# Optimization experiments

Hardware: AMD Instinct MI355X
Metric: run time of the kernel (lower is better)

## Reference

```python
import jax, jax.numpy as jnp
import numpy as np

N = 100000
E = 1600000
C = 128
NEG_SLOPE = 0.2
BN_EPS = 1e-5


def setup_inputs() -> dict:
    key = jax.random.key(0)
    ks = jax.random.split(key, 6)
    x = jax.random.normal(ks[0], (N, C), dtype=jnp.float32)
    edge_index = jax.random.randint(ks[1], (2, E), 0, N, dtype=jnp.int64)
    # Glorot-ish scaled params, stacked over the 3 layers (all 128->128)
    Ws = jax.random.normal(ks[2], (3, C, C), dtype=jnp.float32) * (1.0 / np.sqrt(C))
    att_srcs = jax.random.normal(ks[3], (3, C), dtype=jnp.float32) * (1.0 / np.sqrt(C))
    att_dsts = jax.random.normal(ks[4], (3, C), dtype=jnp.float32) * (1.0 / np.sqrt(C))
    biases = jnp.zeros((3, C), dtype=jnp.float32)
    gammas = jnp.ones((3, C), dtype=jnp.float32)
    betas = jnp.zeros((3, C), dtype=jnp.float32)
    return {"x": x, "edge_index": edge_index, "Ws": Ws, "att_srcs": att_srcs,
            "att_dsts": att_dsts, "biases": biases, "gammas": gammas, "betas": betas}


def _gat_layer(x, W, a_src, a_dst, bias, src, dst):
    # linear transform: [N, C]
    h = x @ W
    # per-node attention logits
    s_src = h @ a_src  # [N]
    s_dst = h @ a_dst  # [N]
    # edge-wise gather + leaky relu scoring
    e = jax.nn.leaky_relu(s_src[src] + s_dst[dst], NEG_SLOPE)  # [E+N]
    # scatter-softmax over incoming edges of each target node
    m = jax.ops.segment_max(e, dst, num_segments=N)  # every node has a self-loop
    ex = jnp.exp(e - m[dst])
    denom = jax.ops.segment_sum(ex, dst, num_segments=N)
    alpha = ex / denom[dst]  # [E+N]
    # scatter-add aggregation of alpha-weighted source features
    out = jax.ops.segment_sum(alpha[:, None] * h[src], dst, num_segments=N)
    return out + bias


def _batch_norm(x, gamma, beta):
    mu = jnp.mean(x, axis=0)
    var = jnp.mean(jnp.square(x - mu), axis=0)
    return gamma * (x - mu) * jax.lax.rsqrt(var + BN_EPS) + beta


def reference(x, edge_index, Ws, att_srcs, att_dsts, biases, gammas, betas):
    # PyG GATConv adds self-loops by default
    loops = jnp.arange(N, dtype=edge_index.dtype)
    src = jnp.concatenate([edge_index[0], loops])
    dst = jnp.concatenate([edge_index[1], loops])
    outs = []
    for l in range(3):
        x = _gat_layer(x, Ws[l], att_srcs[l], att_dsts[l], biases[l], src, dst)
        x = jax.nn.relu(x)
        x = _batch_norm(x, gammas[l], betas[l])
        outs.append(x)
    # jump=True: concat all layer outputs -> [N, 3*C]
    return jnp.concatenate(outs, axis=-1)
```

## Files before the change

### kernel.cpp

```cpp
#include <hip/hip_runtime.h>
#include <math.h>

#define N_NODES 100000
#define N_EDGES 1600000
#define M_TOT   (N_EDGES + N_NODES)
#define C_DIM   128
#define NEG_SLOPE 0.2f
#define BN_EPS 1e-5f

#define NBUCK 8
#define BUCK_NODES 12500
#define BUCK_CAP 240000

#define KS2 72
#define BN_NB 256
#define SCAN_NB 98

typedef _Float16 f16x8 __attribute__((ext_vector_type(8)));
typedef float f32x4 __attribute__((ext_vector_type(4)));

static __device__ __forceinline__ unsigned short f2h(float f) {
    _Float16 h = (_Float16)f;
    unsigned short u;
    __builtin_memcpy(&u, &h, 2);
    return u;
}
static __device__ __forceinline__ float h2f(unsigned short u) {
    _Float16 h;
    __builtin_memcpy(&h, &u, 2);
    return (float)h;
}

__global__ void zero_i32(int* __restrict__ p, int n) {
    int i = blockIdx.x * blockDim.x + threadIdx.x;
    if (i < n) p[i] = 0;
}

__global__ __launch_bounds__(256) void bucket_edges(const int* __restrict__ ei,
                                                    int* __restrict__ bucket_next,
                                                    int2* __restrict__ buckets) {
    __shared__ int cnt[NBUCK];
    __shared__ int base[NBUCK];
    int tid = threadIdx.x;
    if (tid < NBUCK) cnt[tid] = 0;
    __syncthreads();
    int m = blockIdx.x * 256 + tid;
    int src = 0, dst = 0, p = 0, myoff = 0;
    bool valid = (m < M_TOT);
    if (valid) {
        if (m < N_EDGES) { src = ei[m]; dst = ei[N_EDGES + m]; }
        else             { src = m - N_EDGES; dst = src; }
        p = dst / BUCK_NODES;
        myoff = atomicAdd(&cnt[p], 1);
    }
    __syncthreads();
    if (tid < NBUCK) base[tid] = (cnt[tid] > 0) ? atomicAdd(&bucket_next[tid], cnt[tid]) : 0;
    __syncthreads();
    if (valid) {
        buckets[(size_t)p * BUCK_CAP + base[p] + myoff] = make_int2(src, dst);
    }
}

__global__ __launch_bounds__(256) void count_deg_b(const int2* __restrict__ buckets,
                                                   const int* __restrict__ bucket_next,
                                                   int* __restrict__ deg) {
    int p = blockIdx.x & 7;
    int chunk = blockIdx.x >> 3;
    int len = bucket_next[p];
    const int2* b = buckets + (size_t)p * BUCK_CAP;
    int stride = (gridDim.x >> 3) * 256;
    for (int i = chunk * 256 + threadIdx.x; i < len; i += stride) {
        atomicAdd(&deg[b[i].y], 1);
    }
}

__global__ __launch_bounds__(256) void scatter_b(const int2* __restrict__ buckets,
                                                 const int* __restrict__ bucket_next,
                                                 int* __restrict__ nextp,
                                                 int* __restrict__ csr_src) {
    int p = blockIdx.x & 7;
    int chunk = blockIdx.x >> 3;
    int len = bucket_next[p];
    const int2* b = buckets + (size_t)p * BUCK_CAP;
    int stride = (gridDim.x >> 3) * 256;
    for (int i = chunk * 256 + threadIdx.x; i < len; i += stride) {
        int2 e = b[i];
        int pos = atomicAdd(&nextp[e.y], 1);
        csr_src[pos] = e.x;
    }
}

__global__ __launch_bounds__(256) void block_sums(const int* __restrict__ deg,
                                                  int* __restrict__ partials) {
    __shared__ int lds[256];
    int base = blockIdx.x * 1024;
    int s = 0;
    for (int i = threadIdx.x; i < 1024; i += 256) {
        int idx = base + i;
        if (idx < N_NODES) s += deg[idx];
    }
    lds[threadIdx.x] = s;
    __syncthreads();
    for (int off = 128; off > 0; off >>= 1) {
        if (threadIdx.x < off) lds[threadIdx.x] += lds[threadIdx.x + off];
        __syncthreads();
    }
    if (threadIdx.x == 0) partials[blockIdx.x] = lds[0];
}

__global__ __launch_bounds__(128) void scan_partials(int* __restrict__ partials, int nb,
                                                     int* __restrict__ row_ptr) {
    __shared__ int lds[128];
    int tid = threadIdx.x;
    int v = (tid < nb) ? partials[tid] : 0;
    lds[tid] = v;
    __syncthreads();
    for (int off = 1; off < 128; off <<= 1) {
        int t = (tid >= off) ? lds[tid - off] : 0;
        __syncthreads();
        lds[tid] += t;
        __syncthreads();
    }
    if (tid < nb) partials[tid] = lds[tid] - v;
    if (tid == 0) row_ptr[N_NODES] = M_TOT;
}

__global__ __launch_bounds__(256) void scan_write(const int* __restrict__ deg,
                                                  const int* __restrict__ partials,
                                                  int* __restrict__ row_ptr,
                                                  int* __restrict__ nextp) {
    __shared__ int lds[256];
    int tid = threadIdx.x;
    int base = blockIdx.x * 1024;
    int i0 = base + tid * 4;
    int d[4];
#pragma unroll
    for (int t = 0; t < 4; ++t)
        d[t] = (i0 + t < N_NODES) ? deg[i0 + t] : 0;
    int tsum = d[0] + d[1] + d[2] + d[3];
    lds[tid] = tsum;
    __syncthreads();
    for (int off = 1; off < 256; off <<= 1) {
        int v = (tid >= off) ? lds[tid - off] : 0;
        __syncthreads();
        lds[tid] += v;
        __syncthreads();
    }
    int excl = lds[tid] - tsum;
    int run = partials[blockIdx.x] + excl;
#pragma unroll
    for (int t = 0; t < 4; ++t) {
        if (i0 + t < N_NODES) {
            row_ptr[i0 + t] = run;
            nextp[i0 + t]   = run;
            run += d[t];
        }
    }
}

__global__ __launch_bounds__(256, 3) void gemm_attn(
    const float* __restrict__ X, int ldx,
    const float* __restrict__ W,
    const float* __restrict__ a_src, const float* __restrict__ a_dst,
    const float* __restrict__ gbv,
    float* __restrict__ outw,
    unsigned short* __restrict__ Hh, float* __restrict__ Ssrc,
    float* __restrict__ Sdst) {
    __shared__ unsigned short Xs[128 * KS2];
    __shared__ unsigned short Wt[128 * KS2];
    int tid = threadIdx.x;
    int rbase = blockIdx.x * 128;

    int wave = tid >> 6;
    int lane = tid & 63;
    int q = lane >> 4;
    int l15 = lane & 15;
    int wrow = wave * 32;

    f32x4 acc[2][8] = {};

    for (int kb = 0; kb < 128; kb += 64) {
        __syncthreads();
        {
            int rl = tid >> 4;
            int cg = (tid & 15) * 4;
            float4 gg = make_float4(1.f, 1.f, 1.f, 1.f);
            float4 bb = make_float4(0.f, 0.f, 0.f, 0.f);
            if (gbv) {
                gg = *(const float4*)&gbv[kb + cg];
                bb = *(const float4*)&gbv[128 + kb + cg];
            }
#pragma unroll
            for (int i = 0; i < 8; ++i) {
                int r = rl + i * 16;
                int row0 = rbase + r;
                bool ok = (row0 < N_NODES);
                int row = ok ? row0 : (N_NODES - 1);
                float4 v = *(const float4*)&X[(size_t)row * ldx + kb + cg];
                if (gbv) {
                    v.x = fmaf(v.x, gg.x, bb.x);
                    v.y = fmaf(v.y, gg.y, bb.y);
                    v.z = fmaf(v.z, gg.z, bb.z);
                    v.w = fmaf(v.w, gg.w, bb.w);
                    if (ok) *(float4*)&outw[(size_t)row * 384 + kb + cg] = v;
                }
                ushort4 o;
                o.x = f2h(v.x); o.y = f2h(v.y); o.z = f2h(v.z); o.w = f2h(v.w);
                *(ushort4*)&Xs[r * KS2 + cg] = o;
            }
        }
        {
            int kl = tid >> 5;
            int n4 = (tid & 31) * 4;
#pragma unroll
            for (int i = 0; i < 8; ++i) {
                int kk = kl + i * 8;
                float4 v = *(const float4*)&W[(kb + kk) * 128 + n4];
                Wt[(n4 + 0) * KS2 + kk] = f2h(v.x);
                Wt[(n4 + 1) * KS2 + kk] = f2h(v.y);
                Wt[(n4 + 2) * KS2 + kk] = f2h(v.z);
                Wt[(n4 + 3) * KS2 + kk] = f2h(v.w);
            }
        }
        __syncthreads();
#pragma unroll
        for (int ks = 0; ks < 64; ks += 32) {
            int k0 = ks + q * 8;
            f16x8 a0 = *(f16x8*)&Xs[(wrow + l15) * KS2 + k0];
            f16x8 a1 = *(f16x8*)&Xs[(wrow + 16 + l15) * KS2 + k0];
#pragma unroll
            for (int c = 0; c < 8; ++c) {
                f16x8 b = *(f16x8*)&Wt[(c * 16 + l15) * KS2 + k0];
                acc[0][c] = __builtin_amdgcn_mfma_f32_16x16x32_f16(a0, b, acc[0][c], 0, 0, 0);
                acc[1][c] = __builtin_amdgcn_mfma_f32_16x16x32_f16(a1, b, acc[1][c], 0, 0, 0);
            }
        }
    }

    float avs[8], avd[8];
#pragma unroll
    for (int c = 0; c < 8; ++c) {
        avs[c] = a_src[c * 16 + l15];
        avd[c] = a_dst[c * 16 + l15];
    }
#pragma unroll
    for (int r = 0; r < 2; ++r) {
        float ps[4] = {0, 0, 0, 0}, pd[4] = {0, 0, 0, 0};
#pragma unroll
        for (int g = 0; g < 4; ++g) {
            int row = rbase + wrow + r * 16 + q * 4 + g;
            bool ok = (row < N_NODES);
#pragma unroll
            for (int c = 0; c < 8; ++c) {
                float h = acc[r][c][g];
                if (ok) Hh[(size_t)row * 128 + c * 16 + l15] = f2h(h);
                ps[g] = fmaf(h, avs[c], ps[g]);
                pd[g] = fmaf(h, avd[c], pd[g]);
            }
        }
#pragma unroll
        for (int g = 0; g < 4; ++g) {
#pragma unroll
            for (int off = 1; off < 16; off <<= 1) {
                ps[g] += __shfl_xor(ps[g], off, 64);
                pd[g] += __shfl_xor(pd[g], off, 64);
            }
        }
        if (l15 == 0) {
#pragma unroll
            for (int g = 0; g < 4; ++g) {
                int row = rbase + wrow + r * 16 + q * 4 + g;
                if (row < N_NODES) {
                    Ssrc[row] = ps[g];
                    Sdst[row] = pd[g];
                }
            }
        }
    }
}

__global__ __launch_bounds__(256) void aggregate(
    const unsigned short* __restrict__ Hh, const int* __restrict__ row_ptr,
    const int* __restrict__ csr_src,
    const float* __restrict__ Ssrc, const float* __restrict__ Sdst,
    const float* __restrict__ bias, float* __restrict__ Y) {
    int wave = threadIdx.x >> 6;
    int lane = threadIdx.x & 63;
    int g = lane >> 4;
    int l15 = lane & 15;
    int v = blockIdx.x * 4 + wave;
    int start = row_ptr[v];
    int end = row_ptr[v + 1];
    float sdv = Sdst[v];

    float sself = Ssrc[v] + sdv;
    float m = (sself > 0.0f) ? sself : NEG_SLOPE * sself;

    float acc[8] = {0, 0, 0, 0, 0, 0, 0, 0};
    float denom = 0.0f;

    int j = start;
    for (; j + 16 <= end; j += 16) {
        int u0 = csr_src[j + g];
        int u1 = csr_src[j + 4 + g];
        int u2 = csr_src[j + 8 + g];
        int u3 = csr_src[j + 12 + g];
        float ss0 = Ssrc[u0];
        float ss1 = Ssrc[u1];
        float ss2 = Ssrc[u2];
        float ss3 = Ssrc[u3];
        f16x8 h0 = *(const f16x8*)&Hh[(size_t)u0 * 128 + l15 * 8];
        f16x8 h1 = *(const f16x8*)&Hh[(size_t)u1 * 128 + l15 * 8];
        f16x8 h2 = *(const f16x8*)&Hh[(size_t)u2 * 128 + l15 * 8];
        f16x8 h3 = *(const f16x8*)&Hh[(size_t)u3 * 128 + l15 * 8];
        float s0 = ss0 + sdv; s0 = (s0 > 0.0f) ? s0 : NEG_SLOPE * s0;
        float s1 = ss1 + sdv; s1 = (s1 > 0.0f) ? s1 : NEG_SLOPE * s1;
        float s2 = ss2 + sdv; s2 = (s2 > 0.0f) ? s2 : NEG_SLOPE * s2;
        float s3 = ss3 + sdv; s3 = (s3 > 0.0f) ? s3 : NEG_SLOPE * s3;
        float w0 = __expf(s0 - m);
        float w1 = __expf(s1 - m);
        float w2 = __expf(s2 - m);
        float w3 = __expf(s3 - m);
        denom += (w0 + w1) + (w2 + w3);
#pragma unroll
        for (int i = 0; i < 8; ++i) acc[i] = fmaf(w0, (float)h0[i], acc[i]);
#pragma unroll
        for (int i = 0; i < 8; ++i) acc[i] = fmaf(w1, (float)h1[i], acc[i]);
#pragma unroll
        for (int i = 0; i < 8; ++i) acc[i] = fmaf(w2, (float)h2[i], acc[i]);
#pragma unroll
        for (int i = 0; i < 8; ++i) acc[i] = fmaf(w3, (float)h3[i], acc[i]);
    }
    for (; j + 8 <= end; j += 8) {
        int u0 = csr_src[j + g];
        int u1 = csr_src[j + 4 + g];
        float ss0 = Ssrc[u0];
        float ss1 = Ssrc[u1];
        f16x8 h0 = *(const f16x8*)&Hh[(size_t)u0 * 128 + l15 * 8];
        f16x8 h1 = *(const f16x8*)&Hh[(size_t)u1 * 128 + l15 * 8];
        float s0 = ss0 + sdv; s0 = (s0 > 0.0f) ? s0 : NEG_SLOPE * s0;
        float s1 = ss1 + sdv; s1 = (s1 > 0.0f) ? s1 : NEG_SLOPE * s1;
        float w0 = __expf(s0 - m);
        float w1 = __expf(s1 - m);
        denom += w0 + w1;
#pragma unroll
        for (int i = 0; i < 8; ++i) acc[i] = fmaf(w0, (float)h0[i], acc[i]);
#pragma unroll
        for (int i = 0; i < 8; ++i) acc[i] = fmaf(w1, (float)h1[i], acc[i]);
    }
    for (; j < end; j += 4) {
        int je = j + g;
        bool ok = (je < end);
        int u = ok ? csr_src[je] : v;
        float s = Ssrc[u] + sdv; s = (s > 0.0f) ? s : NEG_SLOPE * s;
        float w = ok ? __expf(s - m) : 0.0f;
        f16x8 h = *(const f16x8*)&Hh[(size_t)u * 128 + l15 * 8];
        denom += w;
#pragma unroll
        for (int i = 0; i < 8; ++i) acc[i] = fmaf(w, (float)h[i], acc[i]);
    }

#pragma unroll
    for (int i = 0; i < 8; ++i) {
        acc[i] += __shfl_xor(acc[i], 16, 64);
        acc[i] += __shfl_xor(acc[i], 32, 64);
    }
    denom += __shfl_xor(denom, 16, 64);
    denom += __shfl_xor(denom, 32, 64);

    if (g == 0) {
        float inv = 1.0f / denom;
        float4 b0 = *(const float4*)&bias[l15 * 8];
        float4 b1 = *(const float4*)&bias[l15 * 8 + 4];
        float4 o0, o1;
        o0.x = fmaxf(fmaf(acc[0], inv, b0.x), 0.0f);
        o0.y = fmaxf(fmaf(acc[1], inv, b0.y), 0.0f);
        o0.z = fmaxf(fmaf(acc[2], inv, b0.z), 0.0f);
        o0.w = fmaxf(fmaf(acc[3], inv, b0.w), 0.0f);
        o1.x = fmaxf(fmaf(acc[4], inv, b1.x), 0.0f);
        o1.y = fmaxf(fmaf(acc[5], inv, b1.y), 0.0f);
        o1.z = fmaxf(fmaf(acc[6], inv, b1.z), 0.0f);
        o1.w = fmaxf(fmaf(acc[7], inv, b1.w), 0.0f);
        *(float4*)&Y[(size_t)v * 128 + l15 * 8] = o0;
        *(float4*)&Y[(size_t)v * 128 + l15 * 8 + 4] = o1;
    }
}

__global__ __launch_bounds__(256) void bn_stats(const float* __restrict__ Y,
                                                float* __restrict__ partial) {
    __shared__ float red[256 * 8];
    int tid = threadIdx.x;
    int rowlane = tid >> 5;
    int cg = tid & 31;
    float4 s = make_float4(0, 0, 0, 0);
    float4 qq = make_float4(0, 0, 0, 0);
    for (int i = blockIdx.x * 8 + rowlane; i < N_NODES; i += BN_NB * 8) {
        float4 v = *(const float4*)&Y[(size_t)i * 128 + cg * 4];
        s.x += v.x; s.y += v.y; s.z += v.z; s.w += v.w;
        qq.x = fmaf(v.x, v.x, qq.x);
        qq.y = fmaf(v.y, v.y, qq.y);
        qq.z = fmaf(v.z, v.z, qq.z);
        qq.w = fmaf(v.w, v.w, qq.w);
    }
    float* r = &red[tid * 8];
    r[0] = s.x; r[1] = s.y; r[2] = s.z; r[3] = s.w;
    r[4] = qq.x; r[5] = qq.y; r[6] = qq.z; r[7] = qq.w;
    __syncthreads();
    for (int off = 4; off > 0; off >>= 1) {
        if (rowlane < off) {
            float* o = &red[(tid + off * 32) * 8];
#pragma unroll
            for (int t = 0; t < 8; ++t) r[t] += o[t];
        }
        __syncthreads();
    }
    if (rowlane == 0) {
        *(float4*)&partial[(size_t)blockIdx.x * 256 + cg * 4] =
            make_float4(r[0], r[1], r[2], r[3]);
        *(float4*)&partial[(size_t)blockIdx.x * 256 + 128 + cg * 4] =
            make_float4(r[4], r[5], r[6], r[7]);
    }
}

__global__ __launch_bounds__(256) void bn_finalize(const float* __restrict__ partial,
                                                   const float* __restrict__ gamma,
                                                   const float* __restrict__ beta,
                                                   float* __restrict__ gb) {
    __shared__ float tot[256];
    int tid = threadIdx.x;
    float acc = 0.0f;
    for (int b = 0; b < BN_NB; ++b) acc += partial[(size_t)b * 256 + tid];
    tot[tid] = acc;
    __syncthreads();
    if (tid < 128) {
        const float invN = 1.0f / (float)N_NODES;
        float mu = tot[tid] * invN;
        float var = tot[128 + tid] * invN - mu * mu;
        float g = gamma[tid] * rsqrtf(var + BN_EPS);
        gb[tid] = g;
        gb[128 + tid] = beta[tid] - mu * g;
    }
}

__global__ __launch_bounds__(256) void bn_apply(const float* __restrict__ Y,
                                                const float* __restrict__ gb,
                                                float* __restrict__ out) {
    int idx = blockIdx.x * blockDim.x + threadIdx.x;
    if (idx >= N_NODES * 32) return;
    int row = idx >> 5;
    int c4 = (idx & 31) * 4;
    float4 v = *(const float4*)&Y[(size_t)row * 128 + c4];
    float4 g = *(const float4*)&gb[c4];
    float4 b = *(const float4*)&gb[128 + c4];
    v.x = fmaf(v.x, g.x, b.x);
    v.y = fmaf(v.y, g.y, b.y);
    v.z = fmaf(v.z, g.z, b.z);
    v.w = fmaf(v.w, g.w, b.w);
    *(float4*)&out[(size_t)row * 384 + c4] = v;
}

extern "C" void kernel_launch(void* const* d_in, const int* in_sizes, int n_in,
                              void* d_out, int out_size, void* d_ws, size_t ws_size,
                              hipStream_t stream) {
    const float* x      = (const float*)d_in[0];
    const int*   ei     = (const int*)d_in[1];
    const float* Wall   = (const float*)d_in[2];
    const float* asrcs  = (const float*)d_in[3];
    const float* adsts  = (const float*)d_in[4];
    const float* biases = (const float*)d_in[5];
    const float* gammas = (const float*)d_in[6];
    const float* betas  = (const float*)d_in[7];
    float* out = (float*)d_out;

    unsigned short* Hh = (unsigned short*)d_ws;
    float* Y       = (float*)(Hh + (size_t)N_NODES * 128);
    float* Ssrc    = Y + (size_t)N_NODES * 128;
    float* Sdst    = Ssrc + N_NODES;
    float* bnpart  = Sdst + N_NODES;
    float* gb      = bnpart + BN_NB * 256;
    int* deg       = (int*)(gb + 256);
    int* bucket_next = deg + N_NODES;
    int* row_ptr   = bucket_next + NBUCK;
    int* nextp     = row_ptr + (N_NODES + 1);
    int* partials  = nextp + N_NODES;
    int* csr_src   = partials + 128;
    int2* buckets  = (int2*)(csr_src + M_TOT + 2);

    const int ZERO_CNT = N_NODES + NBUCK;
    const int NB_EDGE = (M_TOT + 255) / 256;
    const int NB_PART = 2048;

    zero_i32<<<(ZERO_CNT + 255) / 256, 256, 0, stream>>>(deg, ZERO_CNT);
    bucket_edges<<<NB_EDGE, 256, 0, stream>>>(ei, bucket_next, buckets);
    count_deg_b<<<NB_PART, 256, 0, stream>>>(buckets, bucket_next, deg);
    block_sums<<<SCAN_NB, 256, 0, stream>>>(deg, partials);
    scan_partials<<<1, 128, 0, stream>>>(partials, SCAN_NB, row_ptr);
    scan_write<<<SCAN_NB, 256, 0, stream>>>(deg, partials, row_ptr, nextp);
    scatter_b<<<NB_PART, 256, 0, stream>>>(buckets, bucket_next, nextp, csr_src);

    for (int l = 0; l < 3; ++l) {
        const float* xin;
        int ldx;
        const float* gbl;
        float* outw;
        if (l == 0) { xin = x; ldx = 128; gbl = nullptr; outw = nullptr; }
        else        { xin = Y; ldx = 128; gbl = gb; outw = out + (size_t)(l - 1) * 128; }
        gemm_attn<<<(N_NODES + 127) / 128, 256, 0, stream>>>(
            xin, ldx, Wall + (size_t)l * 128 * 128,
            asrcs + l * 128, adsts + l * 128, gbl, outw, Hh, Ssrc, Sdst);
        aggregate<<<N_NODES / 4, 256, 0, stream>>>(
            Hh, row_ptr, csr_src, Ssrc, Sdst, biases + l * 128, Y);
        bn_stats<<<BN_NB, 256, 0, stream>>>(Y, bnpart);
        bn_finalize<<<1, 256, 0, stream>>>(bnpart, gammas + l * 128,
                                           betas + l * 128, gb);
    }
    bn_apply<<<(N_NODES * 32 + 255) / 256, 256, 0, stream>>>(
        Y, gb, out + (size_t)2 * 128);
}
```

Before: 803.8 us.

## Pre-convert weights to fp16 and feed MFMA operands directly from global memory

Adds a one-time kernel that converts all three weight matrices to transposed fp16. The GEMM then drops its LDS staging and barriers: each lane loads its X rows straight from global memory into MFMA A-fragments, applying the batch-norm affine inline, and reads B-fragments from the prepacked fp16 weights. This removes shared-memory traffic, the per-block W conversion and transposition, and the synchronisation. In exchange, W reads hit L2/L1 for every wave rather than being reused from LDS, the X loads are less coalesced, and the occupancy hint drops from 3 to 2.

```diff
diff --git a/kernel.cpp b/kernel.cpp
--- a/kernel.cpp
+++ b/kernel.cpp
@@ -12,7 +12,6 @@
 #define BUCK_NODES 12500
 #define BUCK_CAP 240000
 
-#define KS2 72
 #define BN_NB 256
 #define SCAN_NB 98
 
@@ -30,10 +29,22 @@
     __builtin_memcpy(&h, &u, 2);
     return (float)h;
 }
+static __device__ __forceinline__ _Float16 f2h16(float f) { return (_Float16)f; }
 
 __global__ void zero_i32(int* __restrict__ p, int n) {
     int i = blockIdx.x * blockDim.x + threadIdx.x;
     if (i < n) p[i] = 0;
+}
+
+__global__ __launch_bounds__(256) void conv_w(const float* __restrict__ Wall,
+                                              unsigned short* __restrict__ Wh) {
+    int i = blockIdx.x * 256 + threadIdx.x;
+    if (i >= 3 * 128 * 128) return;
+    int l = i >> 14;
+    int r = i & 16383;
+    int k = r >> 7;
+    int n = r & 127;
+    Wh[(size_t)l * 16384 + n * 128 + k] = f2h(Wall[i]);
 }
 
 __global__ __launch_bounds__(256) void bucket_edges(const int* __restrict__ ei,
@@ -158,82 +169,69 @@
     }
 }
 
-__global__ __launch_bounds__(256, 3) void gemm_attn(
+__global__ __launch_bounds__(256, 2) void gemm_attn(
     const float* __restrict__ X, int ldx,
-    const float* __restrict__ W,
+    const unsigned short* __restrict__ Wh,
     const float* __restrict__ a_src, const float* __restrict__ a_dst,
     const float* __restrict__ gbv,
     float* __restrict__ outw,
     unsigned short* __restrict__ Hh, float* __restrict__ Ssrc,
     float* __restrict__ Sdst) {
-    __shared__ unsigned short Xs[128 * KS2];
-    __shared__ unsigned short Wt[128 * KS2];
     int tid = threadIdx.x;
-    int rbase = blockIdx.x * 128;
-
     int wave = tid >> 6;
     int lane = tid & 63;
     int q = lane >> 4;
     int l15 = lane & 15;
     int wrow = wave * 32;
+    int rbase = blockIdx.x * 128;
+
+    int row0 = rbase + wrow + l15;
+    int row1 = row0 + 16;
+    bool ok0 = row0 < N_NODES, ok1 = row1 < N_NODES;
+    int r0c = ok0 ? row0 : (N_NODES - 1);
+    int r1c = ok1 ? row1 : (N_NODES - 1);
 
     f32x4 acc[2][8] = {};
 
-    for (int kb = 0; kb < 128; kb += 64) {
-        __syncthreads();
-        {
-            int rl = tid >> 4;
-            int cg = (tid & 15) * 4;
-            float4 gg = make_float4(1.f, 1.f, 1.f, 1.f);
-            float4 bb = make_float4(0.f, 0.f, 0.f, 0.f);
-            if (gbv) {
-                gg = *(const float4*)&gbv[kb + cg];
-                bb = *(const float4*)&gbv[128 + kb + cg];
+#pragma unroll
+    for (int ks = 0; ks < 128; ks += 32) {
+        int k0 = ks + q * 8;
+        float4 v0 = *(const float4*)&X[(size_t)r0c * ldx + k0];
+        float4 v1 = *(const float4*)&X[(size_t)r0c * ldx + k0 + 4];
+        float4 u0 = *(const float4*)&X[(size_t)r1c * ldx + k0];
+        float4 u1 = *(const float4*)&X[(size_t)r1c * ldx + k0 + 4];
+        if (gbv) {
+            float4 g0 = *(const float4*)&gbv[k0];
+            float4 g1 = *(const float4*)&gbv[k0 + 4];
+            float4 b0 = *(const float4*)&gbv[128 + k0];
+            float4 b1 = *(const float4*)&gbv[128 + k0 + 4];
+            v0.x = fmaf(v0.x, g0.x, b0.x); v0.y = fmaf(v0.y, g0.y, b0.y);
+            v0.z = fmaf(v0.z, g0.z, b0.z); v0.w = fmaf(v0.w, g0.w, b0.w);
+            v1.x = fmaf(v1.x, g1.x, b1.x); v1.y = fmaf(v1.y, g1.y, b1.y);
+            v1.z = fmaf(v1.z, g1.z, b1.z); v1.w = fmaf(v1.w, g1.w, b1.w);
+            u0.x = fmaf(u0.x, g0.x, b0.x); u0.y = fmaf(u0.y, g0.y, b0.y);
+            u0.z = fmaf(u0.z, g0.z, b0.z); u0.w = fmaf(u0.w, g0.w, b0.w);
+            u1.x = fmaf(u1.x, g1.x, b1.x); u1.y = fmaf(u1.y, g1.y, b1.y);
+            u1.z = fmaf(u1.z, g1.z, b1.z); u1.w = fmaf(u1.w, g1.w, b1.w);
+            if (ok0) {
+                *(float4*)&outw[(size_t)row0 * 384 + k0] = v0;
+                *(float4*)&outw[(size_t)row0 * 384 + k0 + 4] = v1;
             }
-#pragma unroll
-            for (int i = 0; i < 8; ++i) {
-                int r = rl + i * 16;
-                int row0 = rbase + r;
-                bool ok = (row0 < N_NODES);
-                int row = ok ? row0 : (N_NODES - 1);
-                float4 v = *(const float4*)&X[(size_t)row * ldx + kb + cg];
-                if (gbv) {
-                    v.x = fmaf(v.x, gg.x, bb.x);
-                    v.y = fmaf(v.y, gg.y, bb.y);
-                    v.z = fmaf(v.z, gg.z, bb.z);
-                    v.w = fmaf(v.w, gg.w, bb.w);
-                    if (ok) *(float4*)&outw[(size_t)row * 384 + kb + cg] = v;
-                }
-                ushort4 o;
-                o.x = f2h(v.x); o.y = f2h(v.y); o.z = f2h(v.z); o.w = f2h(v.w);
-                *(ushort4*)&Xs[r * KS2 + cg] = o;
+            if (ok1) {
+                *(float4*)&outw[(size_t)row1 * 384 + k0] = u0;
+                *(float4*)&outw[(size_t)row1 * 384 + k0 + 4] = u1;
             }
         }
-        {
-            int kl = tid >> 5;
-            int n4 = (tid & 31) * 4;
-#pragma unroll
-            for (int i = 0; i < 8; ++i) {
-                int kk = kl + i * 8;
-                float4 v = *(const float4*)&W[(kb + kk) * 128 + n4];
-                Wt[(n4 + 0) * KS2 + kk] = f2h(v.x);
-                Wt[(n4 + 1) * KS2 + kk] = f2h(v.y);
-                Wt[(n4 + 2) * KS2 + kk] = f2h(v.z);
-                Wt[(n4 + 3) * KS2 + kk] = f2h(v.w);
-            }
-        }
-        __syncthreads();
-#pragma unroll
-        for (int ks = 0; ks < 64; ks += 32) {
-            int k0 = ks + q * 8;
-            f16x8 a0 = *(f16x8*)&Xs[(wrow + l15) * KS2 + k0];
-            f16x8 a1 = *(f16x8*)&Xs[(wrow + 16 + l15) * KS2 + k0];
-#pragma unroll
-            for (int c = 0; c < 8; ++c) {
-                f16x8 b = *(f16x8*)&Wt[(c * 16 + l15) * KS2 + k0];
-                acc[0][c] = __builtin_amdgcn_mfma_f32_16x16x32_f16(a0, b, acc[0][c], 0, 0, 0);
-                acc[1][c] = __builtin_amdgcn_mfma_f32_16x16x32_f16(a1, b, acc[1][c], 0, 0, 0);
-            }
+        f16x8 a0, a1;
+        a0[0] = f2h16(v0.x); a0[1] = f2h16(v0.y); a0[2] = f2h16(v0.z); a0[3] = f2h16(v0.w);
+        a0[4] = f2h16(v1.x); a0[5] = f2h16(v1.y); a0[6] = f2h16(v1.z); a0[7] = f2h16(v1.w);
+        a1[0] = f2h16(u0.x); a1[1] = f2h16(u0.y); a1[2] = f2h16(u0.z); a1[3] = f2h16(u0.w);
+        a1[4] = f2h16(u1.x); a1[5] = f2h16(u1.y); a1[6] = f2h16(u1.z); a1[7] = f2h16(u1.w);
+#pragma unroll
+        for (int c = 0; c < 8; ++c) {
+            f16x8 b = *(const f16x8*)&Wh[(size_t)(c * 16 + l15) * 128 + k0];
+            acc[0][c] = __builtin_amdgcn_mfma_f32_16x16x32_f16(a0, b, acc[0][c], 0, 0, 0);
+            acc[1][c] = __builtin_amdgcn_mfma_f32_16x16x32_f16(a1, b, acc[1][c], 0, 0, 0);
         }
     }
 
@@ -478,7 +476,8 @@
     float* Sdst    = Ssrc + N_NODES;
     float* bnpart  = Sdst + N_NODES;
     float* gb      = bnpart + BN_NB * 256;
-    int* deg       = (int*)(gb + 256);
+    unsigned short* Wh = (unsigned short*)(gb + 256);
+    int* deg       = (int*)(Wh + 3 * 128 * 128);
     int* bucket_next = deg + N_NODES;
     int* row_ptr   = bucket_next + NBUCK;
     int* nextp     = row_ptr + (N_NODES + 1);
@@ -491,6 +490,7 @@
     const int NB_PART = 2048;
 
     zero_i32<<<(ZERO_CNT + 255) / 256, 256, 0, stream>>>(deg, ZERO_CNT);
+    conv_w<<<192, 256, 0, stream>>>(Wall, Wh);
     bucket_edges<<<NB_EDGE, 256, 0, stream>>>(ei, bucket_next, buckets);
     count_deg_b<<<NB_PART, 256, 0, stream>>>(buckets, bucket_next, deg);
     block_sums<<<SCAN_NB, 256, 0, stream>>>(deg, partials);
@@ -506,7 +506,7 @@
         if (l == 0) { xin = x; ldx = 128; gbl = nullptr; outw = nullptr; }
         else        { xin = Y; ldx = 128; gbl = gb; outw = out + (size_t)(l - 1) * 128; }
         gemm_attn<<<(N_NODES + 127) / 128, 256, 0, stream>>>(
-            xin, ldx, Wall + (size_t)l * 128 * 128,
+            xin, ldx, Wh + (size_t)l * 128 * 128,
             asrcs + l * 128, adsts + l * 128, gbl, outw, Hh, Ssrc, Sdst);
         aggregate<<<N_NODES / 4, 256, 0, stream>>>(
             Hh, row_ptr, csr_src, Ssrc, Sdst, biases + l * 128, Y);
```

Result: no change. 792.8 us (-1.4%).
